# Kernel tuning notes

Measured on AMD Instinct MI355X. Metric: run time of the kernel, lower is better.

## Reference

```python
import jax, jax.numpy as jnp
import numpy as np

EPS = 1e-8
N = 1024          # number of points
C = 16            # channels per layer
RBF_LOW, RBF_HIGH, RBF_COUNT = 0.0, 3.5, 32


def _rand(key, shape, scale=0.1):
    return scale * jax.random.normal(key, shape, dtype=jnp.float32)


def setup_inputs() -> dict:
    key = jax.random.key(0)
    ks = jax.random.split(key, 20)
    R = RBF_COUNT
    return {
        'points':   jax.random.normal(ks[0], (N, 3), dtype=jnp.float32),
        # layer 1: 2 radial filters (0->0 and 0->1), output_dim = 1 input channel
        'l1_W1':    _rand(ks[1],  (2, R, R)),
        'l1_B1':    _rand(ks[2],  (2, R)),
        'l1_W2':    _rand(ks[3],  (2, R, 1)),
        'l1_B2':    _rand(ks[4],  (2, 1)),
        'l1_si0_w': _rand(ks[5],  (C, 1)),
        'l1_si0_b': _rand(ks[6],  (C,)),
        'l1_si1_w': _rand(ks[7],  (C, 1)),
        'l1_nl_b':  _rand(ks[8],  (C,)),
        # layer 2: 5 radial filters (0->0, 0->1, 1->0, 1->1 id, 1->1 levi-civita)
        'l2_W1':    _rand(ks[9],  (5, R, R)),
        'l2_B1':    _rand(ks[10], (5, R)),
        'l2_W2':    _rand(ks[11], (5, R, C)),
        'l2_B2':    _rand(ks[12], (5, C)),
        'l2_si0_w': _rand(ks[13], (C, 2 * C)),
        'l2_si0_b': _rand(ks[14], (C,)),
        'l2_si1_w': _rand(ks[15], (C, 3 * C)),
        'l2_nl_b':  _rand(ks[16], (C,)),
        # readout
        'fc_w':     _rand(ks[17], (C, 8)),
        'fc_b':     _rand(ks[18], (8,)),
    }


def _eijk():
    e = np.zeros((3, 3, 3), dtype=np.float32)
    e[0, 1, 2] = e[1, 2, 0] = e[2, 0, 1] = 1.0
    e[0, 2, 1] = e[2, 1, 0] = e[1, 0, 2] = -1.0
    return jnp.asarray(e)


def _norm_eps(x, axis, keepdims=False):
    # norm_with_epsilon: sqrt(max(sum(x^2), EPS))
    return jnp.sqrt(jnp.maximum(jnp.sum(x * x, axis=axis, keepdims=keepdims), EPS))


def _radial(rbf, w1, b1, w2, b2):
    # R(): two-layer relu MLP on rbf features -> [N, N, F]
    h = jax.nn.relu(rbf @ w1 + b1)
    return h @ w2 + b2


def _geometry(points):
    rij = points[:, None, :] - points[None, :, :]          # [N,N,3]
    ss = jnp.sum(rij * rij, axis=-1)                        # [N,N]
    mask0 = ss < EPS                                        # dij == 0 (diagonal)
    dij = jnp.where(mask0, 0.0, jnp.sqrt(jnp.where(mask0, 1.0, ss)))
    centers = jnp.linspace(RBF_LOW, RBF_HIGH, RBF_COUNT, dtype=jnp.float32)
    gamma = jnp.float32(RBF_COUNT / (RBF_HIGH - RBF_LOW))
    rbf = jnp.exp(-gamma * (dij[..., None] - centers) ** 2)  # [N,N,RBF]
    unit = rij / _norm_eps(rij, axis=-1, keepdims=True)       # unit_vectors
    return rbf, unit, mask0


def _F1(rad, unit, mask0):
    # F_1: mask radial where dij==0, multiply by unit vectors -> [N,N,F,3]
    mr = jnp.where(mask0[..., None], 0.0, rad)
    return mr[..., None] * unit[:, :, None, :]


def _nonlinearity(x0, x1, b1):
    # degree-0: pointwise elu; degree-1: norm nonlinearity x * elu(|x|+b)/|x|
    x0 = jax.nn.elu(x0)
    n = _norm_eps(x1, axis=-1)                              # [N,C]
    x1 = x1 * (jax.nn.elu(n + b1) / n)[..., None]
    return x0, x1


def reference(points, l1_W1, l1_B1, l1_W2, l1_B2, l1_si0_w, l1_si0_b, l1_si1_w,
              l1_nl_b, l2_W1, l2_B1, l2_W2, l2_B2, l2_si0_w, l2_si0_b, l2_si1_w,
              l2_nl_b, fc_w, fc_b):
    rbf, unit, mask0 = _geometry(points)
    eijk = _eijk().astype(points.dtype)
    n_pts = points.shape[0]
    x0 = jnp.ones((n_pts, 1, 1), dtype=points.dtype)        # degree-0 input [N,1,1]

    # ---- layer 1: only degree-0 input -> (0->0) and (0->1) filters ----
    r00 = _radial(rbf, l1_W1[0], l1_B1[0], l1_W2[0], l1_B2[0])
    out0 = jnp.einsum('abf,bfi->afi', r00, x0)              # filter_0
    F1a = _F1(_radial(rbf, l1_W1[1], l1_B1[1], l1_W2[1], l1_B2[1]), unit, mask0)
    out1 = jnp.einsum('abfi,bf->afi', F1a, x0[..., 0])
    x0 = jnp.einsum('afi,gf->agi', out0, l1_si0_w) + l1_si0_b[:, None]
    x1 = jnp.einsum('afi,gf->agi', out1, l1_si1_w)
    x0, x1 = _nonlinearity(x0, x1, l1_nl_b)                 # [N,C,1], [N,C,3]

    # ---- layer 2: degree-0 and degree-1 inputs -> 5 filters ----
    rads = [_radial(rbf, l2_W1[i], l2_B1[i], l2_W2[i], l2_B2[i]) for i in range(5)]
    c00 = jnp.einsum('abf,bfi->afi', rads[0], x0)                          # 0x0->0
    c01 = jnp.einsum('abfi,bf->afi', _F1(rads[1], unit, mask0), x0[..., 0])  # 0x1->1
    c10 = jnp.einsum('abfj,bfj->af', _F1(rads[2], unit, mask0), x1)[..., None]  # 1x1->0
    c11 = jnp.einsum('abf,bfi->afi', rads[3], x1)                          # 1x0->1
    c11x = jnp.einsum('ijk,abfj,bfk->afi', eijk, _F1(rads[4], unit, mask0), x1)  # 1x1->1
    cat0 = jnp.concatenate([c00, c10], axis=-2)             # [N,2C,1]
    cat1 = jnp.concatenate([c01, c11, c11x], axis=-2)       # [N,3C,3]
    x0 = jnp.einsum('afi,gf->agi', cat0, l2_si0_w) + l2_si0_b[:, None]
    x1 = jnp.einsum('afi,gf->agi', cat1, l2_si1_w)
    x0, x1 = _nonlinearity(x0, x1, l2_nl_b)

    # ---- readout: invariant degree-0 features, mean-pool over points ----
    g = jnp.mean(x0[..., 0], axis=0)                        # [C]
    return g @ fc_w + fc_b                                  # [num_classes]
```

## Files before the change

kernel.cpp:

```cpp
#include <hip/hip_runtime.h>
#include <hip/hip_bf16.h>
#include <math.h>

#define NP 1024
#define R 32
#define C 16
#define GAMMA (32.0f/3.5f)
#define DC (3.5f/31.0f)

typedef __attribute__((ext_vector_type(8))) short bf16x8;
typedef __attribute__((ext_vector_type(4))) float f32x4;

__device__ __forceinline__ short tobf(float x){
    __hip_bfloat16 h = __float2bfloat16(x);
    return __builtin_bit_cast(short, h);
}
__device__ __forceinline__ float frombf(short s){
    __hip_bfloat16 h = __builtin_bit_cast(__hip_bfloat16, s);
    return __bfloat162float(h);
}
__device__ __forceinline__ unsigned pack2bf(float a, float b){
    const unsigned lo = (unsigned short)tobf(a);
    const unsigned hi = (unsigned short)tobf(b);
    return lo | (hi << 16);
}
__device__ __forceinline__ float eluf(float x){ return x > 0.f ? x : expm1f(x); }

__device__ __forceinline__ f32x4 mfma16(bf16x8 a, bf16x8 b, f32x4 c){
    return __builtin_amdgcn_mfma_f32_16x16x32_bf16(a, b, c, 0, 0, 0);
}

template<int STRIDE>
__device__ __forceinline__ void load_bfrag(const float* __restrict__ src, int q, int n,
                                           bf16x8& hi, bf16x8& lo){
    #pragma unroll
    for (int jj = 0; jj < 8; jj++){
        const float w = src[(q*8+jj)*STRIDE + n];
        const short h = tobf(w);
        hi[jj] = h;
        lo[jj] = tobf(w - frombf(h));
    }
}

__global__ __launch_bounds__(256) void k_layer1(
    const float* __restrict__ points,
    const float* __restrict__ W1, const float* __restrict__ B1,
    const float* __restrict__ W2, const float* __restrict__ B2,
    float* __restrict__ out0, float* __restrict__ out1)
{
    __shared__ float sS0[4][32];
    __shared__ float sT[4][32][3];
    __shared__ float sUp[4][3];

    const int tid  = threadIdx.x;
    const int lane = tid & 63;
    const int wv   = tid >> 6;
    const int l16  = lane & 15;
    const int q    = lane >> 4;
    const int a    = blockIdx.x;
    const float pax = points[a*3+0], pay = points[a*3+1], paz = points[a*3+2];

    bf16x8 w1hi[2][2], w1lo[2][2];
    float  b1v[2][2];
    #pragma unroll
    for (int fi = 0; fi < 2; fi++)
        #pragma unroll
        for (int nt = 0; nt < 2; nt++){
            load_bfrag<R>(W1 + fi*R*R, q, nt*16 + l16, w1hi[fi][nt], w1lo[fi][nt]);
            b1v[fi][nt] = B1[fi*R + nt*16 + l16];
        }

    float s0a[2] = {0.f, 0.f};
    float T[2][3] = {};
    float upx = 0.f, upy = 0.f, upz = 0.f;

    for (int bt = 0; bt < 16; bt++){
        const int bA = bt*64 + wv*16 + l16;
        const float rx = pax - points[bA*3+0];
        const float ry = pay - points[bA*3+1];
        const float rz = paz - points[bA*3+2];
        const float ss = rx*rx + ry*ry + rz*rz;
        const float dij = sqrtf(ss);
        const float inv = 1.0f / sqrtf(fmaxf(ss, 1e-8f));
        const float ux = rx*inv, uy = ry*inv, uz = rz*inv;
        upx += ux; upy += uy; upz += uz;

        bf16x8 afrag;
        #pragma unroll
        for (int jj = 0; jj < 8; jj++){
            const float t = dij - (float)(q*8+jj)*DC;
            afrag[jj] = tobf(__expf(-GAMMA*t*t));
        }

        float uxr[4], uyr[4], uzr[4];
        #pragma unroll
        for (int r4 = 0; r4 < 4; r4++){
            const int sl = q*4 + r4;
            uxr[r4] = __shfl(ux, sl, 16);
            uyr[r4] = __shfl(uy, sl, 16);
            uzr[r4] = __shfl(uz, sl, 16);
        }

        #pragma unroll
        for (int nt = 0; nt < 2; nt++){
            f32x4 c = {b1v[0][nt], b1v[0][nt], b1v[0][nt], b1v[0][nt]};
            c = mfma16(afrag, w1hi[0][nt], c);
            c = mfma16(afrag, w1lo[0][nt], c);
            s0a[nt] += fmaxf(c[0],0.f)+fmaxf(c[1],0.f)+fmaxf(c[2],0.f)+fmaxf(c[3],0.f);
        }
        #pragma unroll
        for (int nt = 0; nt < 2; nt++){
            f32x4 c = {b1v[1][nt], b1v[1][nt], b1v[1][nt], b1v[1][nt]};
            c = mfma16(afrag, w1hi[1][nt], c);
            c = mfma16(afrag, w1lo[1][nt], c);
            #pragma unroll
            for (int r4 = 0; r4 < 4; r4++){
                const float h = fmaxf(c[r4], 0.f);
                T[nt][0] = fmaf(h, uxr[r4], T[nt][0]);
                T[nt][1] = fmaf(h, uyr[r4], T[nt][1]);
                T[nt][2] = fmaf(h, uzr[r4], T[nt][2]);
            }
        }
    }

    #pragma unroll
    for (int nt = 0; nt < 2; nt++){
        s0a[nt] += __shfl_down(s0a[nt], 32, 64);
        s0a[nt] += __shfl_down(s0a[nt], 16, 64);
        #pragma unroll
        for (int i = 0; i < 3; i++){
            T[nt][i] += __shfl_down(T[nt][i], 32, 64);
            T[nt][i] += __shfl_down(T[nt][i], 16, 64);
        }
    }
    #pragma unroll
    for (int off = 32; off > 0; off >>= 1){
        upx += __shfl_down(upx, off, 64);
        upy += __shfl_down(upy, off, 64);
        upz += __shfl_down(upz, off, 64);
    }
    if (lane < 16){
        sS0[wv][lane]      = s0a[0];
        sS0[wv][16 + lane] = s0a[1];
        #pragma unroll
        for (int i = 0; i < 3; i++){
            sT[wv][lane][i]      = T[0][i];
            sT[wv][16 + lane][i] = T[1][i];
        }
    }
    if (lane == 0){ sUp[wv][0] = upx; sUp[wv][1] = upy; sUp[wv][2] = upz; }
    __syncthreads();
    if (tid == 0){
        float o0 = 0.f;
        for (int j = 0; j < R; j++){
            const float S = sS0[0][j] + sS0[1][j] + sS0[2][j] + sS0[3][j];
            o0 = fmaf(S, W2[j], o0);
        }
        out0[a] = o0 + (float)NP * B2[0];
        for (int i = 0; i < 3; i++){
            float t = 0.f;
            for (int j = 0; j < R; j++){
                const float Tj = sT[0][j][i] + sT[1][j][i] + sT[2][j][i] + sT[3][j][i];
                t = fmaf(Tj, W2[R + j], t);
            }
            const float Ui = 0.25f * (sUp[0][i] + sUp[1][i] + sUp[2][i] + sUp[3][i]);
            out1[a*3+i] = t + B2[1] * Ui;
        }
    }
}

__global__ __launch_bounds__(256) void k_point1(
    const float* __restrict__ out0, const float* __restrict__ out1,
    const float* __restrict__ si0_w, const float* __restrict__ si0_b,
    const float* __restrict__ si1_w, const float* __restrict__ nl_b,
    float* __restrict__ x0g, float* __restrict__ x1s)
{
    const int b = blockIdx.x*256 + threadIdx.x;
    if (b >= NP) return;
    const float o0 = out0[b];
    const float o1x = out1[b*3+0], o1y = out1[b*3+1], o1z = out1[b*3+2];
    #pragma unroll
    for (int g = 0; g < C; g++){
        x0g[b*C+g] = eluf(fmaf(o0, si0_w[g], si0_b[g]));
        const float w = si1_w[g];
        const float tx = o1x*w, ty = o1y*w, tz = o1z*w;
        const float n = sqrtf(fmaxf(tx*tx + ty*ty + tz*tz, 1e-8f));
        const float sc = eluf(n + nl_b[g]) / n;
        x1s[0*NP*C + b*C+g] = tx*sc;
        x1s[1*NP*C + b*C+g] = ty*sc;
        x1s[2*NP*C + b*C+g] = tz*sc;
    }
}

__global__ __launch_bounds__(256) void k_layer2(
    const float* __restrict__ points,
    const float* __restrict__ W1, const float* __restrict__ B1,
    const float* __restrict__ W2, const float* __restrict__ B2,
    const float* __restrict__ x0g, const float* __restrict__ x1s,
    float* __restrict__ c00, float* __restrict__ c10)
{
    __shared__ __align__(16) short sH[4][2][16*40];
    __shared__ float sRed[4][2][16];

    const int tid  = threadIdx.x;
    const int lane = tid & 63;
    const int wv   = tid >> 6;
    const int l16  = lane & 15;
    const int q    = lane >> 4;
    const int a    = blockIdx.x;
    const float pax = points[a*3+0], pay = points[a*3+1], paz = points[a*3+2];

    bf16x8 w1hi[2][2], w1lo[2][2], w2hi[2], w2lo[2];
    float  b1v[2][2], b2v[2];
    #pragma unroll
    for (int fi = 0; fi < 2; fi++){
        const int fx = (fi == 0) ? 0 : 2;
        #pragma unroll
        for (int nt = 0; nt < 2; nt++){
            load_bfrag<R>(W1 + fx*R*R, q, 2*l16 + nt, w1hi[fi][nt], w1lo[fi][nt]);
            b1v[fi][nt] = B1[fx*R + 2*l16 + nt];
        }
        load_bfrag<C>(W2 + fx*R*C, q, l16, w2hi[fi], w2lo[fi]);
        b2v[fi] = B2[fx*C + l16];
    }

    float acc0 = 0.f, acc1 = 0.f;
    short* sH0 = sH[wv][0];
    short* sH1 = sH[wv][1];

    for (int bt = 0; bt < 16; bt++){
        const int bA = bt*64 + wv*16 + l16;
        const float rx = pax - points[bA*3+0];
        const float ry = pay - points[bA*3+1];
        const float rz = paz - points[bA*3+2];
        const float ss = rx*rx + ry*ry + rz*rz;
        const float dij = sqrtf(ss);
        const float inv = 1.0f / sqrtf(fmaxf(ss, 1e-8f));
        const float ux = rx*inv, uy = ry*inv, uz = rz*inv;

        float uxr[4], uyr[4], uzr[4];
        #pragma unroll
        for (int r4 = 0; r4 < 4; r4++){
            const int sl = q*4 + r4;
            uxr[r4] = __shfl(ux, sl, 16);
            uyr[r4] = __shfl(uy, sl, 16);
            uzr[r4] = __shfl(uz, sl, 16);
        }

        const int rb = (bt*64 + wv*16 + q*4)*C + l16;
        float x0v[4], udv[4];
        #pragma unroll
        for (int r4 = 0; r4 < 4; r4++){
            x0v[r4] = x0g[rb + r4*C];
            const float v0 = x1s[0*NP*C + rb + r4*C];
            const float v1 = x1s[1*NP*C + rb + r4*C];
            const float v2 = x1s[2*NP*C + rb + r4*C];
            udv[r4] = uxr[r4]*v0 + uyr[r4]*v1 + uzr[r4]*v2;
        }

        bf16x8 afrag;
        #pragma unroll
        for (int jj = 0; jj < 8; jj++){
            const float t = dij - (float)(q*8+jj)*DC;
            afrag[jj] = tobf(__expf(-GAMMA*t*t));
        }

        #pragma unroll
        for (int fi = 0; fi < 2; fi++){
            f32x4 c0 = {b1v[fi][0], b1v[fi][0], b1v[fi][0], b1v[fi][0]};
            c0 = mfma16(afrag, w1hi[fi][0], c0);
            c0 = mfma16(afrag, w1lo[fi][0], c0);
            f32x4 c1 = {b1v[fi][1], b1v[fi][1], b1v[fi][1], b1v[fi][1]};
            c1 = mfma16(afrag, w1hi[fi][1], c1);
            c1 = mfma16(afrag, w1lo[fi][1], c1);
            short* sHf = (fi == 0) ? sH0 : sH1;
            #pragma unroll
            for (int r4 = 0; r4 < 4; r4++){
                const unsigned p = pack2bf(fmaxf(c0[r4], 0.f), fmaxf(c1[r4], 0.f));
                *(unsigned*)&sHf[(q*4+r4)*40 + 2*l16] = p;
            }
        }
        asm volatile("s_waitcnt lgkmcnt(0)" ::: "memory");
        #pragma unroll
        for (int fi = 0; fi < 2; fi++){
            const short* sHf = (fi == 0) ? sH0 : sH1;
            const bf16x8 hf = *(const bf16x8*)(sHf + l16*40 + q*8);
            f32x4 d = {0.f, 0.f, 0.f, 0.f};
            d = mfma16(hf, w2hi[fi], d);
            d = mfma16(hf, w2lo[fi], d);
            #pragma unroll
            for (int r4 = 0; r4 < 4; r4++){
                const float v = d[r4] + b2v[fi];
                if (fi == 0) acc0 = fmaf(v, x0v[r4], acc0);
                else         acc1 = fmaf(v, udv[r4], acc1);
            }
        }
    }

    acc0 += __shfl_down(acc0, 32, 64); acc0 += __shfl_down(acc0, 16, 64);
    acc1 += __shfl_down(acc1, 32, 64); acc1 += __shfl_down(acc1, 16, 64);
    if (lane < 16){ sRed[wv][0][lane] = acc0; sRed[wv][1][lane] = acc1; }
    __syncthreads();
    if (tid < 16)
        c00[a*C + tid] = sRed[0][0][tid] + sRed[1][0][tid] + sRed[2][0][tid] + sRed[3][0][tid];
    else if (tid < 32){
        const int f = tid - 16;
        c10[a*C + f] = sRed[0][1][f] + sRed[1][1][f] + sRed[2][1][f] + sRed[3][1][f];
    }
}

__global__ __launch_bounds__(256) void k_readout1(
    const float* __restrict__ c00, const float* __restrict__ c10,
    const float* __restrict__ si0_w, const float* __restrict__ si0_b,
    float* __restrict__ partial)
{
    __shared__ float sred[4*C];
    const int tid = threadIdx.x;
    const int a = blockIdx.x*256 + tid;
    float v00[C], v10[C];
    #pragma unroll
    for (int f = 0; f < C; f++){ v00[f] = c00[a*C+f]; v10[f] = c10[a*C+f]; }
    float xg[C];
    #pragma unroll
    for (int g = 0; g < C; g++){
        float s = si0_b[g];
        #pragma unroll
        for (int f = 0; f < C; f++) s = fmaf(v00[f], si0_w[g*2*C + f], s);
        #pragma unroll
        for (int f = 0; f < C; f++) s = fmaf(v10[f], si0_w[g*2*C + C + f], s);
        xg[g] = eluf(s);
    }
    #pragma unroll
    for (int off = 32; off > 0; off >>= 1){
        #pragma unroll
        for (int g = 0; g < C; g++) xg[g] += __shfl_down(xg[g], off, 64);
    }
    const int lane = tid & 63, wv = tid >> 6;
    if (lane == 0){
        #pragma unroll
        for (int g = 0; g < C; g++) sred[wv*C + g] = xg[g];
    }
    __syncthreads();
    if (tid < C)
        partial[blockIdx.x*C + tid] =
            sred[tid] + sred[C + tid] + sred[2*C + tid] + sred[3*C + tid];
}

__global__ void k_readout2(const float* __restrict__ partial,
                           const float* __restrict__ fc_w,
                           const float* __restrict__ fc_b,
                           float* __restrict__ out)
{
    const int o = threadIdx.x;
    if (o < 8){
        float s = fc_b[o];
        #pragma unroll
        for (int g = 0; g < C; g++){
            const float m = (partial[g] + partial[C+g] + partial[2*C+g] + partial[3*C+g])
                            * (1.0f / (float)NP);
            s = fmaf(m, fc_w[g*8 + o], s);
        }
        out[o] = s;
    }
}

extern "C" void kernel_launch(void* const* d_in, const int* in_sizes, int n_in,
                              void* d_out, int out_size, void* d_ws, size_t ws_size,
                              hipStream_t stream)
{
    (void)in_sizes; (void)n_in; (void)out_size; (void)ws_size;
    const float* points   = (const float*)d_in[0];
    const float* l1_W1    = (const float*)d_in[1];
    const float* l1_B1    = (const float*)d_in[2];
    const float* l1_W2    = (const float*)d_in[3];
    const float* l1_B2    = (const float*)d_in[4];
    const float* l1_si0_w = (const float*)d_in[5];
    const float* l1_si0_b = (const float*)d_in[6];
    const float* l1_si1_w = (const float*)d_in[7];
    const float* l1_nl_b  = (const float*)d_in[8];
    const float* l2_W1    = (const float*)d_in[9];
    const float* l2_B1    = (const float*)d_in[10];
    const float* l2_W2    = (const float*)d_in[11];
    const float* l2_B2    = (const float*)d_in[12];
    const float* l2_si0_w = (const float*)d_in[13];
    const float* l2_si0_b = (const float*)d_in[14];
    const float* fc_w     = (const float*)d_in[17];
    const float* fc_b     = (const float*)d_in[18];

    float* ws      = (float*)d_ws;
    float* out0    = ws;
    float* out1    = out0 + NP;
    float* x0g     = out1 + NP*3;
    float* x1s     = x0g + NP*C;
    float* c00     = x1s + 3*NP*C;
    float* c10     = c00 + NP*C;
    float* partial = c10 + NP*C;

    k_layer1<<<NP, 256, 0, stream>>>(points, l1_W1, l1_B1, l1_W2, l1_B2, out0, out1);
    k_point1<<<NP/256, 256, 0, stream>>>(out0, out1, l1_si0_w, l1_si0_b, l1_si1_w, l1_nl_b, x0g, x1s);
    k_layer2<<<NP, 256, 0, stream>>>(points, l2_W1, l2_B1, l2_W2, l2_B2, x0g, x1s, c00, c10);
    k_readout1<<<NP/256, 256, 0, stream>>>(c00, c10, l2_si0_w, l2_si0_b, partial);
    k_readout2<<<1, 64, 0, stream>>>(partial, fc_w, fc_b, (float*)d_out);
}
```

Baseline: 172.2 us.

## Fuse five kernels into two with atomic-counter last-block readout

Folds the per-point layer-1 nonlinearity into the layer-1 kernel's epilogue, and folds the layer-2 self-interaction, ELU, mean-pool and final FC into the layer-2 kernel. Pooling goes through atomicAdd on padded partial sums, and the last block, found with a global counter, computes the output. Layer 1 zeroes the partial and counter buffers. This removes three kernel launches and their intermediate global traffic, at the cost of 1024 blocks contending on atomics and a fence/counter handshake.

New measurement: 179.2 us. +4.1%, slower.

```diff
diff --git a/kernel.cpp b/kernel.cpp
--- a/kernel.cpp
+++ b/kernel.cpp
@@ -42,15 +42,19 @@
     }
 }
 
-__global__ __launch_bounds__(256) void k_layer1(
+__global__ __launch_bounds__(256) void k_l1p(
     const float* __restrict__ points,
     const float* __restrict__ W1, const float* __restrict__ B1,
     const float* __restrict__ W2, const float* __restrict__ B2,
-    float* __restrict__ out0, float* __restrict__ out1)
+    const float* __restrict__ si0w, const float* __restrict__ si0b,
+    const float* __restrict__ si1w, const float* __restrict__ nlb,
+    float* __restrict__ x0g, float* __restrict__ x1s,
+    float* __restrict__ partial, unsigned* __restrict__ counter)
 {
     __shared__ float sS0[4][32];
     __shared__ float sT[4][32][3];
     __shared__ float sUp[4][3];
+    __shared__ float sO[4];
 
     const int tid  = threadIdx.x;
     const int lane = tid & 63;
@@ -156,7 +160,7 @@
             const float S = sS0[0][j] + sS0[1][j] + sS0[2][j] + sS0[3][j];
             o0 = fmaf(S, W2[j], o0);
         }
-        out0[a] = o0 + (float)NP * B2[0];
+        sO[0] = o0 + (float)NP * B2[0];
         for (int i = 0; i < 3; i++){
             float t = 0.f;
             for (int j = 0; j < R; j++){
@@ -164,43 +168,44 @@
                 t = fmaf(Tj, W2[R + j], t);
             }
             const float Ui = 0.25f * (sUp[0][i] + sUp[1][i] + sUp[2][i] + sUp[3][i]);
-            out1[a*3+i] = t + B2[1] * Ui;
-        }
-    }
-}
-
-__global__ __launch_bounds__(256) void k_point1(
-    const float* __restrict__ out0, const float* __restrict__ out1,
-    const float* __restrict__ si0_w, const float* __restrict__ si0_b,
-    const float* __restrict__ si1_w, const float* __restrict__ nl_b,
-    float* __restrict__ x0g, float* __restrict__ x1s)
-{
-    const int b = blockIdx.x*256 + threadIdx.x;
-    if (b >= NP) return;
-    const float o0 = out0[b];
-    const float o1x = out1[b*3+0], o1y = out1[b*3+1], o1z = out1[b*3+2];
-    #pragma unroll
-    for (int g = 0; g < C; g++){
-        x0g[b*C+g] = eluf(fmaf(o0, si0_w[g], si0_b[g]));
-        const float w = si1_w[g];
+            sO[1+i] = t + B2[1] * Ui;
+        }
+    }
+    __syncthreads();
+    if (tid < C){
+        const int g = tid;
+        const float o0 = sO[0];
+        const float o1x = sO[1], o1y = sO[2], o1z = sO[3];
+        x0g[a*C+g] = eluf(fmaf(o0, si0w[g], si0b[g]));
+        const float w = si1w[g];
         const float tx = o1x*w, ty = o1y*w, tz = o1z*w;
         const float n = sqrtf(fmaxf(tx*tx + ty*ty + tz*tz, 1e-8f));
-        const float sc = eluf(n + nl_b[g]) / n;
-        x1s[0*NP*C + b*C+g] = tx*sc;
-        x1s[1*NP*C + b*C+g] = ty*sc;
-        x1s[2*NP*C + b*C+g] = tz*sc;
-    }
-}
-
-__global__ __launch_bounds__(256) void k_layer2(
+        const float sc = eluf(n + nlb[g]) / n;
+        x1s[0*NP*C + a*C+g] = tx*sc;
+        x1s[1*NP*C + a*C+g] = ty*sc;
+        x1s[2*NP*C + a*C+g] = tz*sc;
+    }
+    if (a == 0){
+        if (tid < C) partial[tid*16] = 0.f;
+        if (tid == 0) *counter = 0u;
+    }
+}
+
+__global__ __launch_bounds__(256) void k_l2r(
     const float* __restrict__ points,
     const float* __restrict__ W1, const float* __restrict__ B1,
     const float* __restrict__ W2, const float* __restrict__ B2,
     const float* __restrict__ x0g, const float* __restrict__ x1s,
-    float* __restrict__ c00, float* __restrict__ c10)
+    const float* __restrict__ si0w, const float* __restrict__ si0b,
+    const float* __restrict__ fcw, const float* __restrict__ fcb,
+    float* __restrict__ partial, unsigned* __restrict__ counter,
+    float* __restrict__ out)
 {
     __shared__ __align__(16) short sH[4][2][16*40];
     __shared__ float sRed[4][2][16];
+    __shared__ float sC[2][16];
+    __shared__ float sP[16];
+    __shared__ unsigned amLast;
 
     const int tid  = threadIdx.x;
     const int lane = tid & 63;
@@ -301,66 +306,40 @@
     acc1 += __shfl_down(acc1, 32, 64); acc1 += __shfl_down(acc1, 16, 64);
     if (lane < 16){ sRed[wv][0][lane] = acc0; sRed[wv][1][lane] = acc1; }
     __syncthreads();
-    if (tid < 16)
-        c00[a*C + tid] = sRed[0][0][tid] + sRed[1][0][tid] + sRed[2][0][tid] + sRed[3][0][tid];
-    else if (tid < 32){
-        const int f = tid - 16;
-        c10[a*C + f] = sRed[0][1][f] + sRed[1][1][f] + sRed[2][1][f] + sRed[3][1][f];
-    }
-}
-
-__global__ __launch_bounds__(256) void k_readout1(
-    const float* __restrict__ c00, const float* __restrict__ c10,
-    const float* __restrict__ si0_w, const float* __restrict__ si0_b,
-    float* __restrict__ partial)
-{
-    __shared__ float sred[4*C];
-    const int tid = threadIdx.x;
-    const int a = blockIdx.x*256 + tid;
-    float v00[C], v10[C];
-    #pragma unroll
-    for (int f = 0; f < C; f++){ v00[f] = c00[a*C+f]; v10[f] = c10[a*C+f]; }
-    float xg[C];
-    #pragma unroll
-    for (int g = 0; g < C; g++){
-        float s = si0_b[g];
-        #pragma unroll
-        for (int f = 0; f < C; f++) s = fmaf(v00[f], si0_w[g*2*C + f], s);
-        #pragma unroll
-        for (int f = 0; f < C; f++) s = fmaf(v10[f], si0_w[g*2*C + C + f], s);
-        xg[g] = eluf(s);
-    }
-    #pragma unroll
-    for (int off = 32; off > 0; off >>= 1){
-        #pragma unroll
-        for (int g = 0; g < C; g++) xg[g] += __shfl_down(xg[g], off, 64);
-    }
-    const int lane = tid & 63, wv = tid >> 6;
-    if (lane == 0){
-        #pragma unroll
-        for (int g = 0; g < C; g++) sred[wv*C + g] = xg[g];
-    }
-    __syncthreads();
-    if (tid < C)
-        partial[blockIdx.x*C + tid] =
-            sred[tid] + sred[C + tid] + sred[2*C + tid] + sred[3*C + tid];
-}
-
-__global__ void k_readout2(const float* __restrict__ partial,
-                           const float* __restrict__ fc_w,
-                           const float* __restrict__ fc_b,
-                           float* __restrict__ out)
-{
-    const int o = threadIdx.x;
-    if (o < 8){
-        float s = fc_b[o];
-        #pragma unroll
-        for (int g = 0; g < C; g++){
-            const float m = (partial[g] + partial[C+g] + partial[2*C+g] + partial[3*C+g])
-                            * (1.0f / (float)NP);
-            s = fmaf(m, fc_w[g*8 + o], s);
-        }
-        out[o] = s;
+    if (tid < 16){
+        sC[0][tid] = sRed[0][0][tid] + sRed[1][0][tid] + sRed[2][0][tid] + sRed[3][0][tid];
+        sC[1][tid] = sRed[0][1][tid] + sRed[1][1][tid] + sRed[2][1][tid] + sRed[3][1][tid];
+    }
+    __syncthreads();
+    if (tid < C){
+        const int g = tid;
+        float s = si0b[g];
+        #pragma unroll
+        for (int f = 0; f < C; f++) s = fmaf(sC[0][f], si0w[g*2*C + f], s);
+        #pragma unroll
+        for (int f = 0; f < C; f++) s = fmaf(sC[1][f], si0w[g*2*C + C + f], s);
+        atomicAdd(&partial[g*16], eluf(s));
+    }
+    __syncthreads();
+    if (tid == 0){
+        __threadfence();
+        const unsigned prev = atomicAdd(counter, 1u);
+        amLast = (prev == NP - 1u) ? 1u : 0u;
+    }
+    __syncthreads();
+    if (amLast){
+        __threadfence();
+        if (tid < C)
+            sP[tid] = __hip_atomic_load(&partial[tid*16], __ATOMIC_RELAXED,
+                                        __HIP_MEMORY_SCOPE_AGENT);
+        __syncthreads();
+        if (tid < 8){
+            float s = fcb[tid];
+            #pragma unroll
+            for (int g = 0; g < C; g++)
+                s = fmaf(sP[g] * (1.0f / (float)NP), fcw[g*8 + tid], s);
+            out[tid] = s;
+        }
     }
 }
 
@@ -387,18 +366,16 @@
     const float* fc_w     = (const float*)d_in[17];
     const float* fc_b     = (const float*)d_in[18];
 
-    float* ws      = (float*)d_ws;
-    float* out0    = ws;
-    float* out1    = out0 + NP;
-    float* x0g     = out1 + NP*3;
-    float* x1s     = x0g + NP*C;
-    float* c00     = x1s + 3*NP*C;
-    float* c10     = c00 + NP*C;
-    float* partial = c10 + NP*C;
-
-    k_layer1<<<NP, 256, 0, stream>>>(points, l1_W1, l1_B1, l1_W2, l1_B2, out0, out1);
-    k_point1<<<NP/256, 256, 0, stream>>>(out0, out1, l1_si0_w, l1_si0_b, l1_si1_w, l1_nl_b, x0g, x1s);
-    k_layer2<<<NP, 256, 0, stream>>>(points, l2_W1, l2_B1, l2_W2, l2_B2, x0g, x1s, c00, c10);
-    k_readout1<<<NP/256, 256, 0, stream>>>(c00, c10, l2_si0_w, l2_si0_b, partial);
-    k_readout2<<<1, 64, 0, stream>>>(partial, fc_w, fc_b, (float*)d_out);
-}
+    float* ws       = (float*)d_ws;
+    float* x0g      = ws;
+    float* x1s      = x0g + NP*C;
+    float* partial  = x1s + 3*NP*C;
+    unsigned* counter = (unsigned*)(partial + C*16);
+
+    k_l1p<<<NP, 256, 0, stream>>>(points, l1_W1, l1_B1, l1_W2, l1_B2,
+                                  l1_si0_w, l1_si0_b, l1_si1_w, l1_nl_b,
+                                  x0g, x1s, partial, counter);
+    k_l2r<<<NP, 256, 0, stream>>>(points, l2_W1, l2_B1, l2_W2, l2_B2,
+                                  x0g, x1s, l2_si0_w, l2_si0_b,
+                                  fc_w, fc_b, partial, counter, (float*)d_out);
+}
```
